# Kernel optimization log

Measured on AMD Instinct MI355X. Metric: run time of the kernel, lower is better.

The kernel has to match this reference:

```python
import jax, jax.numpy as jnp
import numpy as np

NUM_HEADS = 16
NUM_KV_HEADS = 4
HEAD_DIM = 128
BATCH = 4
SEQ = 2048  # equal per-sequence length; cu_seqlens = arange(BATCH+1)*SEQ


def setup_inputs() -> dict:
    key = jax.random.key(0)
    k1, k2, k3 = jax.random.split(key, 3)
    T = BATCH * SEQ
    q = jax.random.normal(k1, (T, NUM_HEADS * HEAD_DIM), dtype=jnp.float32)
    k = jax.random.normal(k2, (T, NUM_KV_HEADS * HEAD_DIM), dtype=jnp.float32)
    v = jax.random.normal(k3, (T, NUM_KV_HEADS * HEAD_DIM), dtype=jnp.float32)
    cu = jnp.arange(BATCH + 1, dtype=jnp.int32) * SEQ
    return {"q": q, "k": k, "v": v, "cu_seqlens_q": cu, "cu_seqlens_k": cu}


def reference(q, k, v, cu_seqlens_q, cu_seqlens_k):
    # Prefill varlen causal attention with GQA (block_tables=None path).
    # Sequences have equal length, so the ragged batch reshapes to dense [B,S,...].
    B = cu_seqlens_q.shape[0] - 1
    T = q.shape[0]
    S = T // B
    D = HEAD_DIM
    G = NUM_HEADS // NUM_KV_HEADS  # GQA group size
    qh = q.reshape(B, S, NUM_KV_HEADS, G, D)
    kh = k.reshape(B, S, NUM_KV_HEADS, D)
    vh = v.reshape(B, S, NUM_KV_HEADS, D)
    scale = 1.0 / np.sqrt(D).astype(np.float32)  # SDPA scale=None default
    # scores: [B, Hkv, G, Sq, Sk]
    scores = jnp.einsum('bqhgd,bkhd->bhgqk', qh, kh) * scale
    causal = jnp.tril(jnp.ones((S, S), dtype=bool))
    scores = jnp.where(causal, scores, jnp.finfo(scores.dtype).min)
    probs = jax.nn.softmax(scores, axis=-1)
    o = jnp.einsum('bhgqk,bkhd->bqhgd', probs, vh)
    return o.reshape(T, NUM_HEADS * HEAD_DIM)
```

## Files before the change

### kernel.cpp

```cpp
#include <hip/hip_runtime.h>


typedef __attribute__((ext_vector_type(8))) short bs8;
typedef __attribute__((ext_vector_type(16))) float f16x;
typedef __attribute__((ext_vector_type(4))) unsigned int u32x4;
typedef __attribute__((ext_vector_type(4))) unsigned short u16x4;
typedef unsigned short u16;
typedef unsigned int u32;

#define B_ 4
#define S_ 2048
#define HQ_ 16
#define HKV_ 4
#define NQT 16
#define NKT_TOT 32
#define TILE_ELEMS 8192

__device__ __forceinline__ u16 f2bf(float f) {
  u32 u = __float_as_uint(f);
  u += 0x7fffu + ((u >> 16) & 1u);
  return (u16)(u >> 16);
}

__global__ void pack_k(const float* __restrict__ k, u16* __restrict__ kp) {
  int g = blockIdx.x * 256 + threadIdx.x;
  int row = g >> 7;
  int col = (g & 127) << 2;
  int h = col >> 7, d0 = col & 127;
  int b = row >> 11, s = row & 2047;
  int kt = s >> 6, kv = s & 63;
  float4 vv = *(const float4*)(k + (size_t)row * 512 + col);
  int ti = (b * HKV_ + h) * NKT_TOT + kt;
  int e = kv * 128 + (d0 ^ (8 * (kv & 15)));
  u16x4 o;
  o.x = f2bf(vv.x); o.y = f2bf(vv.y); o.z = f2bf(vv.z); o.w = f2bf(vv.w);
  *(u16x4*)(kp + (size_t)ti * TILE_ELEMS + e) = o;
}

__global__ void pack_v(const float* __restrict__ v, u16* __restrict__ vp) {
  __shared__ u16 img[TILE_ELEMS];
  int ti = blockIdx.x;
  int kt = ti & 31;
  int bh = ti >> 5;
  int h = bh & 3, b = bh >> 2;
  int t = threadIdx.x;
#pragma unroll
  for (int p = 0; p < 8; ++p) {
    int t2 = p * 256 + t;
    int kvr = t2 >> 5;
    int d0 = (t2 & 31) << 2;
    float4 vv = *(const float4*)(v + (size_t)(b * S_ + kt * 64 + kvr) * 512 + h * 128 + d0);
    float a[4] = {vv.x, vv.y, vv.z, vv.w};
#pragma unroll
    for (int j = 0; j < 4; ++j) {
      int d = d0 + j;
      img[(d >> 1) * 128 + (d & 1) * 64 + (kvr ^ (8 * ((d >> 1) & 7)))] = f2bf(a[j]);
    }
  }
  __syncthreads();
#pragma unroll
  for (int p = 0; p < 4; ++p) {
    int e0 = (p * 256 + t) * 8;
    *(bs8*)(vp + (size_t)ti * TILE_ELEMS + e0) = *(const bs8*)&img[e0];
  }
}

__device__ __forceinline__ void gl2lds(const u16* g, u16* l) {
  __builtin_amdgcn_global_load_lds((const __attribute__((address_space(1))) void*)g,
                                   (__attribute__((address_space(3))) void*)l,
                                   16, 0, 0);
}

__global__ __launch_bounds__(256, 2) void attn_fwd(
    const float* __restrict__ q, const u16* __restrict__ kp,
    const u16* __restrict__ vp, float* __restrict__ out) {
  __shared__ u16 Ks[TILE_ELEMS];
  __shared__ u16 Vs[TILE_ELEMS];

  const int bx = blockIdx.x;
  const int qt = (NQT - 1) - (bx >> 6);
  const int bh = bx & 63;
  const int b = bh >> 4, hq = bh & 15, hkv = hq >> 2;
  const int w = threadIdx.x >> 6, lane = threadIdx.x & 63;
  const int l31 = lane & 31, hi = lane >> 5;
  const int q0 = qt * 128;
  const float scale2 = 0.08838834764831845f * 1.4426950408889634f;

  bs8 qf[8];
  {
    int row = b * S_ + q0 + w * 32 + l31;
    const float* qrow = q + (size_t)row * 2048 + hq * 128;
#pragma unroll
    for (int ki = 0; ki < 8; ++ki) {
      const float* p0 = qrow + ki * 16 + hi * 8;
      float4 a = *(const float4*)p0;
      float4 c = *(const float4*)(p0 + 4);
      bs8 f;
      f[0] = (short)f2bf(a.x * scale2); f[1] = (short)f2bf(a.y * scale2);
      f[2] = (short)f2bf(a.z * scale2); f[3] = (short)f2bf(a.w * scale2);
      f[4] = (short)f2bf(c.x * scale2); f[5] = (short)f2bf(c.y * scale2);
      f[6] = (short)f2bf(c.z * scale2); f[7] = (short)f2bf(c.w * scale2);
      qf[ki] = f;
    }
  }

  f16x O[4];
#pragma unroll
  for (int dt = 0; dt < 4; ++dt)
#pragma unroll
    for (int e = 0; e < 16; ++e) O[dt][e] = 0.f;
  float m_run = -1e30f, l_run = 0.f;

  const size_t tbase = (size_t)((b * HKV_ + hkv) * NKT_TOT) * TILE_ELEMS;
  const u16* kbase = kp + tbase;
  const u16* vbase = vp + tbase;
  const int nkt = 2 * qt + 2;
  const int myrowmax = q0 + w * 32 + 31;
  const int qpos = q0 + w * 32 + l31;

  const int swzk = 8 * (l31 & 15);
  const int swzv = 8 * ((l31 >> 1) & 7);
  const int vrowbase = (l31 >> 1) * 128 + (l31 & 1) * 64;

  for (int t = 0; t < nkt; ++t) {
    __syncthreads();
    {
      const u16* kg = kbase + (size_t)t * TILE_ELEMS;
      const u16* vg = vbase + (size_t)t * TILE_ELEMS;
#pragma unroll
      for (int j = 0; j < 4; ++j) {
        int c = w * 4 + j;
        gl2lds(kg + c * 512 + lane * 8, &Ks[c * 512]);
        gl2lds(vg + c * 512 + lane * 8, &Vs[c * 512]);
      }
    }
    asm volatile("s_waitcnt vmcnt(0)" ::: "memory");
    __syncthreads();

    if (t * 64 <= myrowmax) {
      f16x Sa[2];
#pragma unroll
      for (int kb = 0; kb < 2; ++kb)
#pragma unroll
        for (int e = 0; e < 16; ++e) Sa[kb][e] = 0.f;

      __builtin_amdgcn_s_setprio(1);
#pragma unroll
      for (int ki = 0; ki < 8; ++ki) {
        int koff = (ki * 16 + hi * 8) ^ swzk;
#pragma unroll
        for (int kb = 0; kb < 2; ++kb) {
          bs8 kf = *(const bs8*)&Ks[(kb * 32 + l31) * 128 + koff];
          Sa[kb] = __builtin_amdgcn_mfma_f32_32x32x16_bf16(kf, qf[ki], Sa[kb], 0, 0, 0);
        }
      }
      __builtin_amdgcn_s_setprio(0);

      if (t >= 2 * qt) {
#pragma unroll
        for (int kb = 0; kb < 2; ++kb)
#pragma unroll
          for (int r = 0; r < 16; ++r) {
            int kvpos = t * 64 + kb * 32 + (r & 3) + 8 * (r >> 2) + 4 * hi;
            if (kvpos > qpos) Sa[kb][r] = -1e30f;
          }
      }

      float tm[8];
#pragma unroll
      for (int r = 0; r < 8; ++r)
        tm[r] = fmaxf(fmaxf(Sa[0][r], Sa[0][r + 8]), fmaxf(Sa[1][r], Sa[1][r + 8]));
#pragma unroll
      for (int s = 4; s > 0; s >>= 1)
#pragma unroll
        for (int r = 0; r < s; ++r) tm[r] = fmaxf(tm[r], tm[r + s]);
      float pmax = fmaxf(tm[0], __shfl_xor(tm[0], 32, 64));

      if (__any(pmax > m_run + 8.0f)) {
        float mnew = fmaxf(m_run, pmax);
        float alpha = exp2f(m_run - mnew);
        m_run = mnew;
        l_run *= alpha;
#pragma unroll
        for (int r = 0; r < 16; ++r) {
          float ar = __shfl(alpha, (r & 3) + 8 * (r >> 2) + 4 * hi, 64);
#pragma unroll
          for (int dt = 0; dt < 4; ++dt) O[dt][r] *= ar;
        }
      }

#pragma unroll
      for (int kb = 0; kb < 2; ++kb)
#pragma unroll
        for (int r = 0; r < 16; ++r) Sa[kb][r] = exp2f(Sa[kb][r] - m_run);
      float ts[8];
#pragma unroll
      for (int r = 0; r < 8; ++r)
        ts[r] = (Sa[0][r] + Sa[0][r + 8]) + (Sa[1][r] + Sa[1][r + 8]);
#pragma unroll
      for (int s = 4; s > 0; s >>= 1)
#pragma unroll
        for (int r = 0; r < s; ++r) ts[r] += ts[r + s];
      l_run += ts[0];

      bs8 pf[2][2];
#pragma unroll
      for (int kb = 0; kb < 2; ++kb) {
        u32 pk_[8];
#pragma unroll
        for (int j = 0; j < 8; ++j) {
          float lo = Sa[kb][2 * j], hif = Sa[kb][2 * j + 1];
          asm("v_cvt_pk_bf16_f32 %0, %1, %2" : "=v"(pk_[j]) : "v"(lo), "v"(hif));
        }
#pragma unroll
        for (int ks = 0; ks < 2; ++ks) {
          auto s0 = __builtin_amdgcn_permlane32_swap((int)pk_[4 * ks], (int)pk_[4 * ks + 2], false, false);
          auto s1 = __builtin_amdgcn_permlane32_swap((int)pk_[4 * ks + 1], (int)pk_[4 * ks + 3], false, false);
          u32x4 fw;
          fw[0] = (u32)s0[0]; fw[1] = (u32)s1[0]; fw[2] = (u32)s0[1]; fw[3] = (u32)s1[1];
          pf[kb][ks] = __builtin_bit_cast(bs8, fw);
        }
      }

      __builtin_amdgcn_s_setprio(1);
#pragma unroll
      for (int dt = 0; dt < 4; ++dt) {
#pragma unroll
        for (int kb = 0; kb < 2; ++kb)
#pragma unroll
          for (int ks = 0; ks < 2; ++ks) {
            int kvoff = (kb * 32 + ks * 16 + hi * 8) ^ swzv;
            bs8 vb = *(const bs8*)&Vs[dt * 2048 + vrowbase + kvoff];
            O[dt] = __builtin_amdgcn_mfma_f32_32x32x16_bf16(pf[kb][ks], vb, O[dt], 0, 0, 0);
          }
      }
      __builtin_amdgcn_s_setprio(0);
    }
  }

  float lt = l_run + __shfl_xor(l_run, 32, 64);
  float inv = 1.0f / lt;
  const int orow0 = b * S_ + q0 + w * 32;
#pragma unroll
  for (int r = 0; r < 16; ++r) {
    int qr = (r & 3) + 8 * (r >> 2) + 4 * hi;
    float li = __shfl(inv, qr, 64);
    float* op = out + (size_t)(orow0 + qr) * 2048 + hq * 128 + l31;
#pragma unroll
    for (int dt = 0; dt < 4; ++dt) op[dt * 32] = O[dt][r] * li;
  }
}

extern "C" void kernel_launch(void* const* d_in, const int* in_sizes, int n_in,
                              void* d_out, int out_size, void* d_ws, size_t ws_size,
                              hipStream_t stream) {
  const float* q = (const float*)d_in[0];
  const float* k = (const float*)d_in[1];
  const float* v = (const float*)d_in[2];
  float* out = (float*)d_out;
  u16* kp = (u16*)d_ws;
  u16* vp = kp + (size_t)B_ * HKV_ * NKT_TOT * TILE_ELEMS;

  pack_k<<<(B_ * S_ * 512 / 4) / 256, 256, 0, stream>>>(k, kp);
  pack_v<<<B_ * HKV_ * NKT_TOT, 256, 0, stream>>>(v, vp);
  attn_fwd<<<B_ * HQ_ * NQT, 256, 0, stream>>>(q, kp, vp, out);
}
```

Baseline: 120.4 us.

## Double-buffer K/V tiles in LDS and pre-pack fragments in MFMA order

The attention kernel now uses two LDS slots for K and V and prefetches tile t+1 with global_load_lds while tile t is being computed. A partial vmcnt wait replaces the full drain. The pack kernels are rewritten to store K and V directly in per-lane MFMA fragment order, so each LDS read becomes a contiguous lane*16-byte access with no swizzle arithmetic. The cost is doubled LDS use (64KB per block), which may limit occupancy at two blocks per CU. The pack_v kernel also now does strided scalar global reads.

```diff
diff --git a/kernel.cpp b/kernel.cpp
--- a/kernel.cpp
+++ b/kernel.cpp
@@ -23,45 +23,50 @@
 }
 
 __global__ void pack_k(const float* __restrict__ k, u16* __restrict__ kp) {
-  int g = blockIdx.x * 256 + threadIdx.x;
-  int row = g >> 7;
-  int col = (g & 127) << 2;
-  int h = col >> 7, d0 = col & 127;
-  int b = row >> 11, s = row & 2047;
-  int kt = s >> 6, kv = s & 63;
-  float4 vv = *(const float4*)(k + (size_t)row * 512 + col);
-  int ti = (b * HKV_ + h) * NKT_TOT + kt;
-  int e = kv * 128 + (d0 ^ (8 * (kv & 15)));
-  u16x4 o;
-  o.x = f2bf(vv.x); o.y = f2bf(vv.y); o.z = f2bf(vv.z); o.w = f2bf(vv.w);
-  *(u16x4*)(kp + (size_t)ti * TILE_ELEMS + e) = o;
-}
-
-__global__ void pack_v(const float* __restrict__ v, u16* __restrict__ vp) {
-  __shared__ u16 img[TILE_ELEMS];
   int ti = blockIdx.x;
   int kt = ti & 31;
   int bh = ti >> 5;
   int h = bh & 3, b = bh >> 2;
-  int t = threadIdx.x;
-#pragma unroll
-  for (int p = 0; p < 8; ++p) {
-    int t2 = p * 256 + t;
-    int kvr = t2 >> 5;
-    int d0 = (t2 & 31) << 2;
-    float4 vv = *(const float4*)(v + (size_t)(b * S_ + kt * 64 + kvr) * 512 + h * 128 + d0);
-    float a[4] = {vv.x, vv.y, vv.z, vv.w};
-#pragma unroll
-    for (int j = 0; j < 4; ++j) {
-      int d = d0 + j;
-      img[(d >> 1) * 128 + (d & 1) * 64 + (kvr ^ (8 * ((d >> 1) & 7)))] = f2bf(a[j]);
-    }
-  }
-  __syncthreads();
 #pragma unroll
   for (int p = 0; p < 4; ++p) {
-    int e0 = (p * 256 + t) * 8;
-    *(bs8*)(vp + (size_t)ti * TILE_ELEMS + e0) = *(const bs8*)&img[e0];
+    int s = p * 256 + threadIdx.x;
+    int c = s >> 6, l = s & 63;
+    int kb = c >> 3, ki = c & 7;
+    int kv = kb * 32 + (l & 31);
+    int d0 = ki * 16 + (l >> 5) * 8;
+    const float* src = k + (size_t)(b * S_ + kt * 64 + kv) * 512 + h * 128 + d0;
+    float4 a = *(const float4*)src;
+    float4 cc = *(const float4*)(src + 4);
+    u16* dst = kp + (size_t)ti * TILE_ELEMS + s * 8;
+    u16x4 lo, hi2;
+    lo.x = f2bf(a.x); lo.y = f2bf(a.y); lo.z = f2bf(a.z); lo.w = f2bf(a.w);
+    hi2.x = f2bf(cc.x); hi2.y = f2bf(cc.y); hi2.z = f2bf(cc.z); hi2.w = f2bf(cc.w);
+    *(u16x4*)dst = lo;
+    *(u16x4*)(dst + 4) = hi2;
+  }
+}
+
+__global__ void pack_v(const float* __restrict__ v, u16* __restrict__ vp) {
+  int ti = blockIdx.x;
+  int kt = ti & 31;
+  int bh = ti >> 5;
+  int h = bh & 3, b = bh >> 2;
+#pragma unroll
+  for (int p = 0; p < 4; ++p) {
+    int s = p * 256 + threadIdx.x;
+    int c = s >> 6, l = s & 63;
+    int dt = c >> 2, kb = (c >> 1) & 1, ks = c & 1;
+    int d = dt * 32 + (l & 31);
+    int kv0 = kb * 32 + ks * 16 + (l >> 5) * 8;
+    const float* src = v + (size_t)(b * S_ + kt * 64 + kv0) * 512 + h * 128 + d;
+    u16x4 lo, hi2;
+    lo.x = f2bf(src[0]);          lo.y = f2bf(src[512]);
+    lo.z = f2bf(src[1024]);       lo.w = f2bf(src[1536]);
+    hi2.x = f2bf(src[2048]);      hi2.y = f2bf(src[2560]);
+    hi2.z = f2bf(src[3072]);      hi2.w = f2bf(src[3584]);
+    u16* dst = vp + (size_t)ti * TILE_ELEMS + s * 8;
+    *(u16x4*)dst = lo;
+    *(u16x4*)(dst + 4) = hi2;
   }
 }
 
@@ -74,8 +79,7 @@
 __global__ __launch_bounds__(256, 2) void attn_fwd(
     const float* __restrict__ q, const u16* __restrict__ kp,
     const u16* __restrict__ vp, float* __restrict__ out) {
-  __shared__ u16 Ks[TILE_ELEMS];
-  __shared__ u16 Vs[TILE_ELEMS];
+  __shared__ u16 Sh[2 * 2 * TILE_ELEMS];
 
   const int bx = blockIdx.x;
   const int qt = (NQT - 1) - (bx >> 6);
@@ -118,26 +122,31 @@
   const int myrowmax = q0 + w * 32 + 31;
   const int qpos = q0 + w * 32 + l31;
 
-  const int swzk = 8 * (l31 & 15);
-  const int swzv = 8 * ((l31 >> 1) & 7);
-  const int vrowbase = (l31 >> 1) * 128 + (l31 & 1) * 64;
+#define STAGE(t_, slot_)                                                     \
+  {                                                                          \
+    const u16* kg_ = kbase + (size_t)(t_) * TILE_ELEMS;                      \
+    const u16* vg_ = vbase + (size_t)(t_) * TILE_ELEMS;                      \
+    _Pragma("unroll") for (int j = 0; j < 4; ++j) {                          \
+      int c_ = w * 4 + j;                                                    \
+      gl2lds(kg_ + c_ * 512 + lane * 8, &Sh[(slot_) * 16384 + c_ * 512]);    \
+      gl2lds(vg_ + c_ * 512 + lane * 8, &Sh[(slot_) * 16384 + 8192 + c_ * 512]); \
+    }                                                                        \
+  }
+
+  STAGE(0, 0);
 
   for (int t = 0; t < nkt; ++t) {
-    __syncthreads();
-    {
-      const u16* kg = kbase + (size_t)t * TILE_ELEMS;
-      const u16* vg = vbase + (size_t)t * TILE_ELEMS;
-#pragma unroll
-      for (int j = 0; j < 4; ++j) {
-        int c = w * 4 + j;
-        gl2lds(kg + c * 512 + lane * 8, &Ks[c * 512]);
-        gl2lds(vg + c * 512 + lane * 8, &Vs[c * 512]);
-      }
+    if (t + 1 < nkt) {
+      STAGE(t + 1, (t + 1) & 1);
+      asm volatile("s_waitcnt vmcnt(8)" ::: "memory");
+    } else {
+      asm volatile("s_waitcnt vmcnt(0)" ::: "memory");
     }
-    asm volatile("s_waitcnt vmcnt(0)" ::: "memory");
-    __syncthreads();
+    __builtin_amdgcn_s_barrier();
 
     if (t * 64 <= myrowmax) {
+      const char* lbase = (const char*)Sh + ((t & 1) << 15) + (size_t)lane * 16;
+
       f16x Sa[2];
 #pragma unroll
       for (int kb = 0; kb < 2; ++kb)
@@ -147,10 +156,9 @@
       __builtin_amdgcn_s_setprio(1);
 #pragma unroll
       for (int ki = 0; ki < 8; ++ki) {
-        int koff = (ki * 16 + hi * 8) ^ swzk;
 #pragma unroll
         for (int kb = 0; kb < 2; ++kb) {
-          bs8 kf = *(const bs8*)&Ks[(kb * 32 + l31) * 128 + koff];
+          bs8 kf = *(const bs8*)(lbase + (kb * 8 + ki) * 1024);
           Sa[kb] = __builtin_amdgcn_mfma_f32_32x32x16_bf16(kf, qf[ki], Sa[kb], 0, 0, 0);
         }
       }
@@ -229,13 +237,14 @@
         for (int kb = 0; kb < 2; ++kb)
 #pragma unroll
           for (int ks = 0; ks < 2; ++ks) {
-            int kvoff = (kb * 32 + ks * 16 + hi * 8) ^ swzv;
-            bs8 vb = *(const bs8*)&Vs[dt * 2048 + vrowbase + kvoff];
+            bs8 vb = *(const bs8*)(lbase + 16384 + (dt * 4 + kb * 2 + ks) * 1024);
             O[dt] = __builtin_amdgcn_mfma_f32_32x32x16_bf16(pf[kb][ks], vb, O[dt], 0, 0, 0);
           }
       }
       __builtin_amdgcn_s_setprio(0);
     }
+
+    __builtin_amdgcn_s_barrier();
   }
 
   float lt = l_run + __shfl_xor(l_run, 32, 64);
@@ -261,7 +270,7 @@
   u16* kp = (u16*)d_ws;
   u16* vp = kp + (size_t)B_ * HKV_ * NKT_TOT * TILE_ELEMS;
 
-  pack_k<<<(B_ * S_ * 512 / 4) / 256, 256, 0, stream>>>(k, kp);
+  pack_k<<<B_ * HKV_ * NKT_TOT, 256, 0, stream>>>(k, kp);
   pack_v<<<B_ * HKV_ * NKT_TOT, 256, 0, stream>>>(v, vp);
   attn_fwd<<<B_ * HQ_ * NQT, 256, 0, stream>>>(q, kp, vp, out);
 }
```

New measurement: 122.4 us. No clear change (+1.7%).
